# Kernel optimization log

Hardware: AMD Instinct MI355X
Metric: run time of the kernel (lower is better)

The kernel has to match this reference:

```python
import jax, jax.numpy as jnp
import numpy as np

TAU = 1.0        # gumbel-softmax temperature
H = 8            # n_heads
RD = 32          # routing_dim


def setup_inputs() -> dict:
    key = jax.random.key(0)
    k1, k2, k3, k4, k5 = jax.random.split(key, 5)
    B, T, C = 2, 2048, 1024
    x = jax.random.normal(k1, (B, T, C), dtype=jnp.float32)
    # base adjacency [H,T,T]; keep diagonal free so each causal row has a finite logit
    base_mask = jax.random.randint(k2, (H, T, T), 0, 2).astype(bool)
    base_mask = base_mask & ~jnp.eye(T, dtype=bool)[None]
    # pre-sampled standard Gumbel noise (matches F.gumbel_softmax internals)
    u = jax.random.uniform(k3, (B, H, T, T), dtype=jnp.float32, minval=1e-9, maxval=1.0)
    gumbel = -jnp.log(-jnp.log(u))
    scale = 1.0 / np.sqrt(C).astype(np.float32)
    Wq = jax.random.normal(k4, (C, H * RD), dtype=jnp.float32) * scale
    Wk = jax.random.normal(k5, (C, H * RD), dtype=jnp.float32) * scale
    return {"x": x, "base_mask": base_mask, "gumbel": gumbel, "Wq": Wq, "Wk": Wk}


def reference(x, base_mask, gumbel, Wq, Wk):
    B, T, C = x.shape
    # routing projections -> [B,T,H,RD]
    sq = (x @ Wq).reshape(B, T, H, RD)
    sk = (x @ Wk).reshape(B, T, H, RD)
    # pairwise edge scores [B,H,T,T]
    scores = jnp.einsum("bihd,bjhd->bhij", sq, sk) / np.sqrt(RD).astype(np.float32)
    # causal mask (j > i) OR already-connected base edges -> -inf
    causal = jnp.triu(jnp.ones((T, T), dtype=bool), 1)
    mask = causal[None, None] | base_mask[None]
    scores = jnp.where(mask, -jnp.inf, scores)
    # gumbel-softmax (training path, hard=False): softmax((logits + g) / tau)
    return jax.nn.softmax((scores + gumbel) / TAU, axis=-1)
```

## Files before the change

kernel.cpp:

```cpp
#include <hip/hip_runtime.h>
#include <hip/hip_bf16.h>
#include <math.h>

#define TT    2048
#define HH    8
#define RDIM  32
#define BB    2

typedef float  f4  __attribute__((ext_vector_type(4)));
typedef int    i4  __attribute__((ext_vector_type(4)));
typedef uint   u2  __attribute__((ext_vector_type(2)));
typedef short  s8v __attribute__((ext_vector_type(8)));

__device__ __forceinline__ uint rnd16(float x) {
    return (__float_as_uint(x) + 0x8000u) >> 16;
}

__global__ __launch_bounds__(256) void proj_gemm(
    const float* __restrict__ x,
    const float* __restrict__ Wq,
    const float* __restrict__ Wk,
    ushort* __restrict__ sqb,
    ushort* __restrict__ skb)
{
    constexpr int BK = 32;
    constexpr int LDA = 68;
    constexpr int LDB = 68;
    __shared__ float As[BK][LDA];
    __shared__ float Bs[BK][LDB];

    const int m0 = blockIdx.x * 64;
    const int n0 = blockIdx.y * 64;
    const float* W = (n0 < 256) ? Wq : Wk;
    const int nloc = n0 & 255;

    const int tid = threadIdx.x;
    const int tx = tid & 15;
    const int ty = tid >> 4;

    float acc[4][4] = {};

    for (int k0 = 0; k0 < 1024; k0 += BK) {
        #pragma unroll
        for (int l = 0; l < 2; ++l) {
            int vid = tid + l * 256;
            int row = vid >> 3;
            int cc  = vid & 7;
            f4 v = *(const f4*)&x[(size_t)(m0 + row) * 1024 + k0 + cc * 4];
            As[cc * 4 + 0][row] = v.x;
            As[cc * 4 + 1][row] = v.y;
            As[cc * 4 + 2][row] = v.z;
            As[cc * 4 + 3][row] = v.w;
        }
        #pragma unroll
        for (int l = 0; l < 2; ++l) {
            int vid = tid + l * 256;
            int kr = vid >> 4;
            int c4 = vid & 15;
            f4 v = *(const f4*)&W[(size_t)(k0 + kr) * 256 + nloc + c4 * 4];
            *(f4*)&Bs[kr][c4 * 4] = v;
        }
        __syncthreads();

        #pragma unroll
        for (int k = 0; k < BK; ++k) {
            const f4 a4 = *(const f4*)&As[k][ty * 4];
            const f4 b4 = *(const f4*)&Bs[k][tx * 4];
            float a[4] = {a4.x, a4.y, a4.z, a4.w};
            float bb[4] = {b4.x, b4.y, b4.z, b4.w};
            #pragma unroll
            for (int r = 0; r < 4; ++r)
                #pragma unroll
                for (int c = 0; c < 4; ++c)
                    acc[r][c] = fmaf(a[r], bb[c], acc[r][c]);
        }
        __syncthreads();
    }

    #pragma unroll
    for (int rr = 0; rr < 4; ++rr) {
        int m = m0 + ty * 4 + rr;
        u2 pk;
        pk.x = (rnd16(acc[rr][1]) << 16) | rnd16(acc[rr][0]);
        pk.y = (rnd16(acc[rr][3]) << 16) | rnd16(acc[rr][2]);
        int nn = n0 + tx * 4;
        if (nn < 256) {
            *(u2*)&sqb[(size_t)m * 256 + nn] = pk;
        } else {
            *(u2*)&skb[(size_t)m * 256 + (nn - 256)] = pk;
        }
    }
}

__global__ __launch_bounds__(512) void score_mfma(
    const ushort* __restrict__ sqb,
    const ushort* __restrict__ skb,
    const float*  __restrict__ gumbel,
    const int*    __restrict__ mask,
    float* __restrict__ out)
{
    const int tid = threadIdx.x;
    const int l   = tid & 63;
    const int w   = __builtin_amdgcn_readfirstlane(tid) >> 6;
    const int bh  = blockIdx.x & 15;
    const int sp  = blockIdx.x >> 4;
    const int h   = bh & (HH - 1);
    const int b   = bh >> 3;
    const int cl  = l & 15;
    const int g4  = l >> 4;
    const float RS = 0.17677669529663687f;

    __shared__ float sums_lds[8][16];

    const ushort* sqbase = sqb + ((size_t)b * TT) * 256 + h * RDIM + g4 * 8;
    const ushort* skbase = skb + ((size_t)b * TT) * 256 + h * RDIM + g4 * 8;
    const float*  gb = gumbel + (size_t)bh * TT * TT;
    const int*    mb = mask + (size_t)h * TT * TT;
    float*        ob = out + (size_t)bh * TT * TT;

    #pragma unroll 1
    for (int half = 0; half < 2; ++half) {
        const int s      = half ? (127 - sp) : sp;
        const int i0     = s * 16;
        const int ntiles = s + 1;
        const int zstart = ntiles * 16;
        const int i      = i0 + cl;

        s8v bfrag = *(const s8v*)(sqbase + (size_t)i * 256);

        const float* grow = gb + (size_t)i * TT;
        const int*   mrow = mb + (size_t)i * TT;
        float*       orow = ob + (size_t)i * TT;

        float sum = 0.f;
        u2 p[8][2];
        #pragma unroll
        for (int it = 0; it < 8; ++it) {
            const int jt0 = 2 * w + it * 16;
            #pragma unroll
            for (int u = 0; u < 2; ++u) {
                const int jt = jt0 + u;
                if (jt < ntiles) {
                    s8v afrag = *(const s8v*)(skbase + (size_t)(jt * 16 + cl) * 256);
                    f4 z = {0.f, 0.f, 0.f, 0.f};
                    f4 c = __builtin_amdgcn_mfma_f32_16x16x32_bf16(
                               afrag, bfrag, z, 0, 0, 0);
                    const int jb = jt * 16 + g4 * 4;
                    f4 gv = *(const f4*)&grow[jb];
                    i4 mv = *(const i4*)&mrow[jb];
                    float e0 = (jb + 0 > i || mv.x) ? 0.f : __expf(fmaf(c[0], RS, gv.x));
                    float e1 = (jb + 1 > i || mv.y) ? 0.f : __expf(fmaf(c[1], RS, gv.y));
                    float e2 = (jb + 2 > i || mv.z) ? 0.f : __expf(fmaf(c[2], RS, gv.z));
                    float e3 = (jb + 3 > i || mv.w) ? 0.f : __expf(fmaf(c[3], RS, gv.w));
                    sum += (e0 + e1) + (e2 + e3);
                    p[it][u].x = (rnd16(e1) << 16) | rnd16(e0);
                    p[it][u].y = (rnd16(e3) << 16) | rnd16(e2);
                }
            }
        }

        sum += __shfl_xor(sum, 16);
        sum += __shfl_xor(sum, 32);
        if (l < 16) sums_lds[w][l] = sum;
        __syncthreads();
        float t = 0.f;
        #pragma unroll
        for (int ww = 0; ww < 8; ++ww) t += sums_lds[ww][cl];
        const float rinv = 1.0f / t;
        __syncthreads();

        #pragma unroll
        for (int it = 0; it < 8; ++it) {
            const int jt0 = 2 * w + it * 16;
            #pragma unroll
            for (int u = 0; u < 2; ++u) {
                const int jt = jt0 + u;
                if (jt < ntiles) {
                    const int jb = jt * 16 + g4 * 4;
                    f4 v;
                    v.x = __uint_as_float(p[it][u].x << 16) * rinv;
                    v.y = __uint_as_float(p[it][u].x & 0xffff0000u) * rinv;
                    v.z = __uint_as_float(p[it][u].y << 16) * rinv;
                    v.w = __uint_as_float(p[it][u].y & 0xffff0000u) * rinv;
                    __builtin_nontemporal_store(v, (f4*)&orow[jb]);
                }
            }
        }

        for (int r = 0; r < 16; ++r) {
            for (int cz = zstart + tid * 4; cz < TT; cz += 512 * 4) {
                f4 zz = {0.f, 0.f, 0.f, 0.f};
                __builtin_nontemporal_store(zz, (f4*)&ob[(size_t)(i0 + r) * TT + cz]);
            }
        }
    }
}

extern "C" void kernel_launch(void* const* d_in, const int* in_sizes, int n_in,
                              void* d_out, int out_size, void* d_ws, size_t ws_size,
                              hipStream_t stream) {
    const float* x      = (const float*)d_in[0];
    const int*   bmask  = (const int*)d_in[1];
    const float* gumbel = (const float*)d_in[2];
    const float* Wq     = (const float*)d_in[3];
    const float* Wk     = (const float*)d_in[4];
    float* out = (float*)d_out;

    ushort* sqb = (ushort*)d_ws;
    ushort* skb = sqb + (size_t)4096 * 256;

    proj_gemm<<<dim3(64, 8), 256, 0, stream>>>(x, Wq, Wk, sqb, skb);

    score_mfma<<<1024, 512, 0, stream>>>(sqb, skb, gumbel, bmask, out);
}
```

Baseline: 190.7 us.

## Replace FP32 projection GEMM with bf16 MFMA using pre-transposed weights

Adds a prep kernel that transposes Wq/Wk into a bf16 [N,K] layout. The scalar FP32 LDS-tiled projection GEMM is replaced by a bf16 MFMA kernel that loads x directly from global memory and converts it to bf16 on the fly. The aim is to cut the time of the projection stage, at the cost of an extra launch and bf16 rounding of x and W. The score kernel's output stores also switch from nontemporal to regular stores, which changes cache behaviour on the large output writes.

```diff
diff --git a/kernel.cpp b/kernel.cpp
--- a/kernel.cpp
+++ b/kernel.cpp
@@ -10,85 +10,108 @@
 typedef float  f4  __attribute__((ext_vector_type(4)));
 typedef int    i4  __attribute__((ext_vector_type(4)));
 typedef uint   u2  __attribute__((ext_vector_type(2)));
+typedef uint   u4  __attribute__((ext_vector_type(4)));
 typedef short  s8v __attribute__((ext_vector_type(8)));
 
 __device__ __forceinline__ uint rnd16(float x) {
     return (__float_as_uint(x) + 0x8000u) >> 16;
 }
 
-__global__ __launch_bounds__(256) void proj_gemm(
-    const float* __restrict__ x,
+union v8cast { u4 u; s8v s; };
+
+__global__ __launch_bounds__(256) void wt_prep(
     const float* __restrict__ Wq,
     const float* __restrict__ Wk,
+    ushort* __restrict__ Wt)
+{
+    __shared__ float T[64][68];
+    const int k0 = blockIdx.x * 64;
+    const int n0 = blockIdx.y * 64;
+    const float* W = (n0 < 256) ? Wq : Wk;
+    const int nloc = n0 & 255;
+    const int tid = threadIdx.x;
+
+    #pragma unroll
+    for (int r = 0; r < 4; ++r) {
+        int kl  = (tid >> 4) + r * 16;
+        int nl4 = (tid & 15) * 4;
+        f4 v = *(const f4*)&W[(size_t)(k0 + kl) * 256 + nloc + nl4];
+        T[nl4 + 0][kl] = v.x;
+        T[nl4 + 1][kl] = v.y;
+        T[nl4 + 2][kl] = v.z;
+        T[nl4 + 3][kl] = v.w;
+    }
+    __syncthreads();
+
+    const int nl = tid >> 2;
+    const int kq = (tid & 3) * 16;
+    u4 o0, o1;
+    #pragma unroll
+    for (int j = 0; j < 4; ++j) {
+        uint lo = rnd16(T[nl][kq + 2 * j]);
+        uint hi = rnd16(T[nl][kq + 2 * j + 1]);
+        ((uint*)&o0)[j] = (hi << 16) | lo;
+    }
+    #pragma unroll
+    for (int j = 0; j < 4; ++j) {
+        uint lo = rnd16(T[nl][kq + 8 + 2 * j]);
+        uint hi = rnd16(T[nl][kq + 8 + 2 * j + 1]);
+        ((uint*)&o1)[j] = (hi << 16) | lo;
+    }
+    ushort* dst = Wt + (size_t)(n0 + nl) * 1024 + k0 + kq;
+    *(u4*)dst = o0;
+    *(u4*)(dst + 8) = o1;
+}
+
+__global__ __launch_bounds__(256) void proj_mfma(
+    const float* __restrict__ x,
+    const ushort* __restrict__ Wt,
     ushort* __restrict__ sqb,
     ushort* __restrict__ skb)
 {
-    constexpr int BK = 32;
-    constexpr int LDA = 68;
-    constexpr int LDB = 68;
-    __shared__ float As[BK][LDA];
-    __shared__ float Bs[BK][LDB];
-
-    const int m0 = blockIdx.x * 64;
-    const int n0 = blockIdx.y * 64;
-    const float* W = (n0 < 256) ? Wq : Wk;
-    const int nloc = n0 & 255;
-
     const int tid = threadIdx.x;
-    const int tx = tid & 15;
-    const int ty = tid >> 4;
-
-    float acc[4][4] = {};
-
-    for (int k0 = 0; k0 < 1024; k0 += BK) {
-        #pragma unroll
-        for (int l = 0; l < 2; ++l) {
-            int vid = tid + l * 256;
-            int row = vid >> 3;
-            int cc  = vid & 7;
-            f4 v = *(const f4*)&x[(size_t)(m0 + row) * 1024 + k0 + cc * 4];
-            As[cc * 4 + 0][row] = v.x;
-            As[cc * 4 + 1][row] = v.y;
-            As[cc * 4 + 2][row] = v.z;
-            As[cc * 4 + 3][row] = v.w;
-        }
-        #pragma unroll
-        for (int l = 0; l < 2; ++l) {
-            int vid = tid + l * 256;
-            int kr = vid >> 4;
-            int c4 = vid & 15;
-            f4 v = *(const f4*)&W[(size_t)(k0 + kr) * 256 + nloc + c4 * 4];
-            *(f4*)&Bs[kr][c4 * 4] = v;
-        }
-        __syncthreads();
-
-        #pragma unroll
-        for (int k = 0; k < BK; ++k) {
-            const f4 a4 = *(const f4*)&As[k][ty * 4];
-            const f4 b4 = *(const f4*)&Bs[k][tx * 4];
-            float a[4] = {a4.x, a4.y, a4.z, a4.w};
-            float bb[4] = {b4.x, b4.y, b4.z, b4.w};
-            #pragma unroll
-            for (int r = 0; r < 4; ++r)
-                #pragma unroll
-                for (int c = 0; c < 4; ++c)
-                    acc[r][c] = fmaf(a[r], bb[c], acc[r][c]);
-        }
-        __syncthreads();
-    }
-
-    #pragma unroll
-    for (int rr = 0; rr < 4; ++rr) {
-        int m = m0 + ty * 4 + rr;
+    const int l   = tid & 63;
+    const int w   = __builtin_amdgcn_readfirstlane(tid) >> 6;
+    const int cl  = l & 15;
+    const int g4  = l >> 4;
+    const int m0  = (blockIdx.x * 4 + w) * 16;
+    const int n0  = blockIdx.y * 64;
+
+    f4 acc0 = {0,0,0,0}, acc1 = {0,0,0,0}, acc2 = {0,0,0,0}, acc3 = {0,0,0,0};
+
+    const float*  xrow = x + (size_t)(m0 + cl) * 1024;
+    const ushort* wbase = Wt + (size_t)(n0 + cl) * 1024;
+
+    for (int ks = 0; ks < 32; ++ks) {
+        const int k = ks * 32 + g4 * 8;
+        f4 xa = *(const f4*)&xrow[k];
+        f4 xb2 = *(const f4*)&xrow[k + 4];
+        v8cast bf;
+        ((uint*)&bf.u)[0] = (rnd16(xa.y) << 16) | rnd16(xa.x);
+        ((uint*)&bf.u)[1] = (rnd16(xa.w) << 16) | rnd16(xa.z);
+        ((uint*)&bf.u)[2] = (rnd16(xb2.y) << 16) | rnd16(xb2.x);
+        ((uint*)&bf.u)[3] = (rnd16(xb2.w) << 16) | rnd16(xb2.z);
+        s8v a0 = *(const s8v*)(wbase + 0 * 16 * 1024 + k);
+        s8v a1 = *(const s8v*)(wbase + 1 * 16 * 1024 + k);
+        s8v a2 = *(const s8v*)(wbase + 2 * 16 * 1024 + k);
+        s8v a3 = *(const s8v*)(wbase + 3 * 16 * 1024 + k);
+        acc0 = __builtin_amdgcn_mfma_f32_16x16x32_bf16(a0, bf.s, acc0, 0, 0, 0);
+        acc1 = __builtin_amdgcn_mfma_f32_16x16x32_bf16(a1, bf.s, acc1, 0, 0, 0);
+        acc2 = __builtin_amdgcn_mfma_f32_16x16x32_bf16(a2, bf.s, acc2, 0, 0, 0);
+        acc3 = __builtin_amdgcn_mfma_f32_16x16x32_bf16(a3, bf.s, acc3, 0, 0, 0);
+    }
+
+    const int m = m0 + cl;
+    const int nbase = n0 + g4 * 4;
+    ushort* obase = (n0 < 256) ? (sqb + (size_t)m * 256 + nbase)
+                               : (skb + (size_t)m * 256 + (nbase - 256));
+    f4 accs[4] = {acc0, acc1, acc2, acc3};
+    #pragma unroll
+    for (int t = 0; t < 4; ++t) {
         u2 pk;
-        pk.x = (rnd16(acc[rr][1]) << 16) | rnd16(acc[rr][0]);
-        pk.y = (rnd16(acc[rr][3]) << 16) | rnd16(acc[rr][2]);
-        int nn = n0 + tx * 4;
-        if (nn < 256) {
-            *(u2*)&sqb[(size_t)m * 256 + nn] = pk;
-        } else {
-            *(u2*)&skb[(size_t)m * 256 + (nn - 256)] = pk;
-        }
+        pk.x = (rnd16(accs[t][1]) << 16) | rnd16(accs[t][0]);
+        pk.y = (rnd16(accs[t][3]) << 16) | rnd16(accs[t][2]);
+        *(u2*)(obase + t * 16) = pk;
     }
 }
 
@@ -182,7 +205,7 @@
                     v.y = __uint_as_float(p[it][u].x & 0xffff0000u) * rinv;
                     v.z = __uint_as_float(p[it][u].y << 16) * rinv;
                     v.w = __uint_as_float(p[it][u].y & 0xffff0000u) * rinv;
-                    __builtin_nontemporal_store(v, (f4*)&orow[jb]);
+                    *(f4*)&orow[jb] = v;
                 }
             }
         }
@@ -190,7 +213,7 @@
         for (int r = 0; r < 16; ++r) {
             for (int cz = zstart + tid * 4; cz < TT; cz += 512 * 4) {
                 f4 zz = {0.f, 0.f, 0.f, 0.f};
-                __builtin_nontemporal_store(zz, (f4*)&ob[(size_t)(i0 + r) * TT + cz]);
+                *(f4*)&ob[(size_t)(i0 + r) * TT + cz] = zz;
             }
         }
     }
@@ -208,8 +231,11 @@
 
     ushort* sqb = (ushort*)d_ws;
     ushort* skb = sqb + (size_t)4096 * 256;
-
-    proj_gemm<<<dim3(64, 8), 256, 0, stream>>>(x, Wq, Wk, sqb, skb);
+    ushort* Wt  = skb + (size_t)4096 * 256;
+
+    wt_prep<<<dim3(16, 8), 256, 0, stream>>>(Wq, Wk, Wt);
+
+    proj_mfma<<<dim3(64, 8), 256, 0, stream>>>(x, Wt, sqb, skb);
 
     score_mfma<<<1024, 512, 0, stream>>>(sqb, skb, gumbel, bmask, out);
 }
```

Result: no change. 187.8 us (-1.5%).
